# Performance work log

Hardware: AMD Instinct MI355X
Metric: run time of the kernel (lower is better)

## Reference

```python
import jax, jax.numpy as jnp
import numpy as np

B, T, C, N = 4, 1024, 1024, 64
H = C // N
# dims = [max(32, 32*round(fac*C**p/32))] per module formula for C=1024
D_W, D_A, D_V, D_G = 64, 64, 32, 160
GN_EPS = 0.00064


def setup_inputs() -> dict:
    key = jax.random.key(0)
    keys = iter(jax.random.split(key, 40))

    def rn(shape, s=0.02):
        return jax.random.normal(next(keys), shape, jnp.float32) * s

    return {
        "x": jax.random.normal(next(keys), (B, T, C), jnp.float32),
        "v_first": jax.random.normal(next(keys), (B, T, C), jnp.float32),
        "x_r": rn((1, 1, C), 0.5), "x_w": rn((1, 1, C), 0.5), "x_k": rn((1, 1, C), 0.5),
        "x_v": rn((1, 1, C), 0.5), "x_a": rn((1, 1, C), 0.5), "x_g": rn((1, 1, C), 0.5),
        "w0": rn((1, 1, C), 0.5) - 1.0, "w1": rn((C, D_W)), "w2": rn((D_W, C)),
        "a0": rn((1, 1, C), 0.5), "a1": rn((C, D_A)), "a2": rn((D_A, C)),
        "v0p": rn((1, 1, C), 0.5), "v1": rn((C, D_V)), "v2": rn((D_V, C)),
        "g1": rn((C, D_G)), "g2": rn((D_G, C)),
        "k_k": rn((1, 1, C), 0.2) + 0.8, "k_a": rn((1, 1, C), 0.2) + 1.0,
        "r_k": rn((H, N), 0.5),
        "W_r": rn((C, C)), "W_k": rn((C, C)), "W_v": rn((C, C)), "W_o": rn((C, C)),
        "gn_w": jnp.ones((C,), jnp.float32), "gn_b": jnp.zeros((C,), jnp.float32),
    }


def _group_norm(x2, wgt, bias):
    # torch GroupNorm(H groups, C channels) on [B*T, C]: normalize each N-chunk
    xg = x2.reshape(x2.shape[0], H, N)
    mu = xg.mean(-1, keepdims=True)
    var = ((xg - mu) ** 2).mean(-1, keepdims=True)  # biased var, as torch
    xn = (xg - mu) * jax.lax.rsqrt(var + GN_EPS)
    return xn.reshape(x2.shape) * wgt + bias


def rwkv7_recurrence(r, w, k, v, a, b):
    # RWKV-7 chunked-cuda semantics (wind_rwkv naive reference), all [B,T,H,N];
    # w is the per-channel decay exp(-exp(w_raw)) in (0,1).
    # state s: [B,H,N,N], s[i,j] ~ value_i x key_j
    # s_t = s_{t-1} * diag(w_t) + (s_{t-1} @ a_t) outer b_t + v_t outer k_t
    # y_t = s_t @ r_t
    def step(s, inp):
        r_t, w_t, k_t, v_t, a_t, b_t = inp  # each [B,H,N]
        sa = jnp.einsum('bhij,bhj->bhi', s, a_t)
        s = (s * w_t[:, :, None, :]
             + sa[..., None] * b_t[:, :, None, :]
             + v_t[..., None] * k_t[:, :, None, :])
        y = jnp.einsum('bhij,bhj->bhi', s, r_t)
        return s, y

    xs = tuple(jnp.swapaxes(t, 0, 1) for t in (r, w, k, v, a, b))  # [T,B,H,N]
    s0 = jnp.zeros((r.shape[0], r.shape[2], r.shape[3], r.shape[3]), r.dtype)
    _, ys = jax.lax.scan(step, s0, xs)
    return jnp.swapaxes(ys, 0, 1)  # [B,T,H,N]


def reference(x, v_first, x_r, x_w, x_k, x_v, x_a, x_g, w0, w1, w2, a0, a1, a2,
              v0p, v1, v2, g1, g2, k_k, k_a, r_k, W_r, W_k, W_v, W_o, gn_w, gn_b):
    Bx, Tx, Cx = x.shape
    # F.pad(x, (0,0,1,-1)): shift tokens right by one, zero at t=0
    last_x = jnp.concatenate([jnp.zeros_like(x[:, :1]), x[:, :-1]], axis=1)
    dx = last_x - x
    xr, xw, xk, xv, xa, xg = (x + m * dx for m in (x_r, x_w, x_k, x_v, x_a, x_g))
    r = xr @ W_r.T
    w = -jax.nn.softplus(-w0 - jnp.tanh(xw @ w1) @ w2) - 0.5
    k = xk @ W_k.T
    v = xv @ W_v.T
    v = v + (v_first - v) * jax.nn.sigmoid(v0p + (xv @ v1) @ v2)
    a = jax.nn.sigmoid(a0 + (xa @ a1) @ a2)
    g = jax.nn.sigmoid(xg @ g1) @ g2
    kk = k * k_k
    k = k * (1.0 + (a - 1.0) * k_a)
    rs, ws, ks, vs, kks, aa = (t.reshape(Bx, Tx, H, N) for t in (r, w, k, v, kk, a))
    # F.normalize(kk, dim=-1) with eps clamp 1e-12
    kks = kks / jnp.maximum(jnp.linalg.norm(kks, axis=-1, keepdims=True), 1e-12)
    wdec = jnp.exp(-jnp.exp(ws))
    y = rwkv7_recurrence(rs, wdec, ks, vs, kks, -kks * aa)  # [B,T,H,N]
    yn = _group_norm(y.reshape(Bx * Tx, Cx), gn_w, gn_b).reshape(Bx, Tx, Cx)
    yn = yn + ((rs * ks * r_k).sum(-1, keepdims=True) * vs).reshape(Bx, Tx, Cx)
    return (yn * g) @ W_o.T
```

## Files before the change

### kernel.cpp

```cpp
#include <hip/hip_runtime.h>
#include <hip/hip_bf16.h>
#include <math.h>


using bf16 = __hip_bfloat16;
typedef __attribute__((ext_vector_type(8))) short bf16x8;
typedef __attribute__((ext_vector_type(4))) float f32x4;

#define DEVINL __device__ __forceinline__

DEVINL float b2f(bf16 v) { return __bfloat162float(v); }
DEVINL bf16 f2b(float f) { return __float2bfloat16(f); }
DEVINL float sigm(float x) { return 1.f / (1.f + __expf(-x)); }
DEVINL float bfbits2f(unsigned short s) { return __uint_as_float(((unsigned)s) << 16); }
DEVINL float ldin(const void* p, size_t i, int fl) {
  return fl ? ((const float*)p)[i] : b2f(((const bf16*)p)[i]);
}

DEVINL void g2lds16(const void* g, void* l) {
  __builtin_amdgcn_global_load_lds(
      (__attribute__((address_space(1))) void*)(g),
      (__attribute__((address_space(3))) void*)(l), 16, 0, 0);
}

template<int CTRL>
DEVINL float dpp_add(float x) {
  int t = __builtin_amdgcn_update_dpp(0, __float_as_int(x), CTRL, 0xf, 0xf, true);
  return x + __int_as_float(t);
}
DEVINL float rowsum32(float x) {
  x = dpp_add<0x121>(x);
  x = dpp_add<0x122>(x);
  x = dpp_add<0x124>(x);
  x = dpp_add<0x128>(x);
  int t = __builtin_amdgcn_ds_swizzle(__float_as_int(x), 0x401F);
  return x + __int_as_float(t);
}

__global__ void detect_kernel(const unsigned* __restrict__ x, int* __restrict__ flag) {
  __shared__ int cnt[4];
  int tid = threadIdx.x;
  unsigned w = x[tid];
  float v = fabsf(bfbits2f((unsigned short)(w & 0xffffu)));
  bool plaus = (v >= 1e-4f && v <= 16.f);
  unsigned long long m = __ballot(plaus);
  if ((tid & 63) == 0) cnt[tid >> 6] = __popcll(m);
  __syncthreads();
  if (tid == 0) *flag = (cnt[0] + cnt[1] + cnt[2] + cnt[3] < 128) ? 1 : 0;
}

__global__ __launch_bounds__(256)
void prep_kernel(const void* __restrict__ x,
    const void* mr, const void* mw, const void* mk,
    const void* mv, const void* ma, const void* mg,
    const void* W_r, const void* W_k, const void* W_v, const void* W_o,
    bf16* cWr, bf16* cWk, bf16* cWv, bf16* cWo,
    const void* w1, const void* w2, const void* a1, const void* a2,
    const void* v1, const void* v2, const void* g1, const void* g2,
    bf16* w1t, bf16* w2t, bf16* a1t, bf16* a2t,
    bf16* v1t, bf16* v2t, bf16* g1t, bf16* g2t,
    const int* __restrict__ flag,
    bf16* oxr, bf16* oxw, bf16* oxk, bf16* oxv, bf16* oxa, bf16* oxg)
{
  int fl = *flag;
  int bx = blockIdx.x;
  if (bx < 16384) {
    size_t idx = (size_t)bx * 256 + threadIdx.x;
    int c = (int)(idx & 1023);
    int t = (int)((idx >> 10) & 1023);
    float xc = ldin(x, idx, fl);
    float px = (t == 0) ? 0.f : ldin(x, idx - 1024, fl);
    float dx = px - xc;
    oxr[idx] = f2b(xc + ldin(mr, c, fl) * dx);
    oxw[idx] = f2b(xc + ldin(mw, c, fl) * dx);
    oxk[idx] = f2b(xc + ldin(mk, c, fl) * dx);
    oxv[idx] = f2b(xc + ldin(mv, c, fl) * dx);
    oxa[idx] = f2b(xc + ldin(ma, c, fl) * dx);
    oxg[idx] = f2b(xc + ldin(mg, c, fl) * dx);
  } else if (bx < 32768) {
    int g = (bx - 16384) * 256 + threadIdx.x;
    int seg = g >> 20, i = g & 1048575;
    const void* s = seg == 0 ? W_r : seg == 1 ? W_k : seg == 2 ? W_v : W_o;
    bf16* d = seg == 0 ? cWr : seg == 1 ? cWk : seg == 2 ? cWv : cWo;
    d[i] = fl ? f2b(((const float*)s)[i]) : ((const bf16*)s)[i];
  } else {
    int idx = (bx - 32768) * 256 + threadIdx.x;
    if (idx >= 655360) return;
    const int ends[8] = {65536, 131072, 196608, 262144, 294912, 327680, 491520, 655360};
    const int Ks[8] = {1024, 64, 1024, 64, 1024, 32, 1024, 160};
    const int Nd[8] = {64, 1024, 64, 1024, 32, 1024, 160, 1024};
    const void* srcs[8] = {w1, w2, a1, a2, v1, v2, g1, g2};
    bf16* dsts[8] = {w1t, w2t, a1t, a2t, v1t, v2t, g1t, g2t};
    int seg = 0, start = 0;
#pragma unroll
    for (int s2 = 0; s2 < 7; s2++)
      if (idx >= ends[s2]) { seg = s2 + 1; start = ends[s2]; }
    int local = idx - start;
    int K = Ks[seg], N = Nd[seg];
    int k = local / N, n = local - k * N;
    dsts[seg][(size_t)n * K + k] = f2b(ldin(srcs[seg], local, fl));
  }
}

template<typename Epi>
DEVINL void gemm_core(const bf16* __restrict__ A, const bf16* __restrict__ Bt,
                      int K, int Brows, int m0, int n0, Epi&& epi)
{
  __shared__ short As[128 * 32];
  __shared__ short Bs[128 * 32];
  const int tid = threadIdx.x;
  const int wid = tid >> 6, lane = tid & 63;
  const int wr = (wid >> 1) * 64, wc = (wid & 1) * 64;

  f32x4 acc[4][4] = {};

  const int lrow = lane >> 2;
  const int lcol = (lane & 3) * 8;
  int arow0 = m0 + (wid * 2 + 0) * 16 + lrow;
  int arow1 = m0 + (wid * 2 + 1) * 16 + lrow;
  int brow0 = n0 + (wid * 2 + 0) * 16 + lrow; if (brow0 >= Brows) brow0 = Brows - 1;
  int brow1 = n0 + (wid * 2 + 1) * 16 + lrow; if (brow1 >= Brows) brow1 = Brows - 1;

  const short* Ag = (const short*)A;
  const short* Bg = (const short*)Bt;

  for (int kk = 0; kk < K; kk += 32) {
    __syncthreads();
    g2lds16(Ag + (size_t)arow0 * K + kk + lcol, As + (wid * 2 + 0) * 512);
    g2lds16(Ag + (size_t)arow1 * K + kk + lcol, As + (wid * 2 + 1) * 512);
    g2lds16(Bg + (size_t)brow0 * K + kk + lcol, Bs + (wid * 2 + 0) * 512);
    g2lds16(Bg + (size_t)brow1 * K + kk + lcol, Bs + (wid * 2 + 1) * 512);
    __syncthreads();
    bf16x8 af[4], bfr[4];
#pragma unroll
    for (int mi = 0; mi < 4; mi++)
      af[mi] = *(const bf16x8*)(As + (wr + mi * 16 + (lane & 15)) * 32 + (lane >> 4) * 8);
#pragma unroll
    for (int ni = 0; ni < 4; ni++)
      bfr[ni] = *(const bf16x8*)(Bs + (wc + ni * 16 + (lane & 15)) * 32 + (lane >> 4) * 8);
#pragma unroll
    for (int mi = 0; mi < 4; mi++)
#pragma unroll
      for (int ni = 0; ni < 4; ni++)
        acc[mi][ni] = __builtin_amdgcn_mfma_f32_16x16x32_bf16(af[mi], bfr[ni], acc[mi][ni], 0, 0, 0);
  }

  const int cl0 = lane & 15, r0 = (lane >> 4) * 4;
#pragma unroll
  for (int mi = 0; mi < 4; mi++)
#pragma unroll
    for (int ni = 0; ni < 4; ni++) {
      int col = n0 + wc + ni * 16 + cl0;
#pragma unroll
      for (int rr = 0; rr < 4; rr++)
        epi(m0 + wr + mi * 16 + r0 + rr, col, acc[mi][ni][rr]);
    }
}

__global__ __launch_bounds__(256)
void stage1_kernel(const bf16* xw, const bf16* xa, const bf16* xv, const bf16* xg,
                   const bf16* w1t, const bf16* a1t, const bf16* v1t, const bf16* g1t,
                   bf16* hw, bf16* ha, bf16* hv, bf16* hg)
{
  int y = blockIdx.y;
  int seg = (y <= 2) ? y : 3;
  int n0 = (y == 4) ? 128 : 0;
  const bf16* A  = seg == 0 ? xw  : seg == 1 ? xa  : seg == 2 ? xv  : xg;
  const bf16* Bt = seg == 0 ? w1t : seg == 1 ? a1t : seg == 2 ? v1t : g1t;
  int NS         = seg == 0 ? 64  : seg == 1 ? 64  : seg == 2 ? 32  : 160;
  bf16* out      = seg == 0 ? hw  : seg == 1 ? ha  : seg == 2 ? hv  : hg;
  gemm_core(A, Bt, 1024, NS, blockIdx.x * 128, n0, [&](int row, int col, float f) {
    if (col >= NS) return;
    if (seg == 0) f = tanhf(f);
    else if (seg == 3) f = sigm(f);
    out[(size_t)row * NS + col] = f2b(f);
  });
}

__global__ __launch_bounds__(256)
void bigrkv_kernel(const bf16* xr, const bf16* xk, const bf16* xv,
                   const bf16* cWr, const bf16* cWk, const bf16* cWv,
                   bf16* __restrict__ PKb)
{
  int z = blockIdx.z;
  const bf16* A  = z == 0 ? xr  : z == 1 ? xk  : xv;
  const bf16* Bt = z == 0 ? cWr : z == 1 ? cWk : cWv;
  gemm_core(A, Bt, 1024, 1024, blockIdx.x * 128, blockIdx.y * 128,
            [&](int row, int col, float f) {
    PKb[(size_t)row * 5120 + (col >> 6) * 320 + z * 64 + (col & 63)] = f2b(f);
  });
}

__global__ __launch_bounds__(256)
void stage2_kernel(const bf16* hw, const bf16* ha, const bf16* hv, const bf16* hg,
                   const bf16* w2t, const bf16* a2t, const bf16* v2t, const bf16* g2t,
                   bf16* __restrict__ PKb, float* __restrict__ PKw, float* __restrict__ G,
                   const void* w0, const void* a0, const void* v0p, const void* vfirst,
                   const int* __restrict__ flag)
{
  int fl = *flag;
  int z = blockIdx.z;
  const bf16* A  = z == 0 ? hw  : z == 1 ? ha  : z == 2 ? hv  : hg;
  const bf16* Bt = z == 0 ? w2t : z == 1 ? a2t : z == 2 ? v2t : g2t;
  int K          = z == 0 ? 64  : z == 1 ? 64  : z == 2 ? 32  : 160;
  gemm_core(A, Bt, K, 1024, blockIdx.x * 128, blockIdx.y * 128,
            [&](int row, int col, float f) {
    if (z == 0) {
      float zz = -(ldin(w0, col, fl) + f);
      float sp = fmaxf(zz, 0.f) + __logf(1.f + __expf(-fabsf(zz)));
      PKw[(size_t)row * 1024 + col] = __expf(-__expf(-sp - 0.5f));
    } else if (z == 1) {
      PKb[(size_t)row * 5120 + (col >> 6) * 320 + 192 + (col & 63)] =
          f2b(sigm(ldin(a0, col, fl) + f));
    } else if (z == 2) {
      float sg = sigm(ldin(v0p, col, fl) + f);
      size_t pa = (size_t)row * 5120 + (col >> 6) * 320 + 128 + (col & 63);
      float vr = b2f(PKb[pa]);
      float vf = ldin(vfirst, (size_t)row * 1024 + col, fl);
      PKb[pa] = f2b(vr + (vf - vr) * sg);
    } else {
      G[(size_t)row * 1024 + col] = f;
    }
  });
}

__global__ __launch_bounds__(256)
void post_kernel(bf16* __restrict__ PKb, const void* __restrict__ kkw,
                 const void* __restrict__ kaw, const int* __restrict__ flag) {
  int fl = *flag;
  int slot = blockIdx.x * 4 + (threadIdx.x >> 6);
  int tg = slot >> 4, h = slot & 15;
  int n = threadIdx.x & 63, c = h * 64 + n;
  size_t pb = (size_t)tg * 5120 + (size_t)h * 320;
  float kraw = b2f(PKb[pb + 64 + n]);
  float asig = b2f(PKb[pb + 192 + n]);
  float kk = kraw * ldin(kkw, c, fl);
  float ss = kk * kk;
  ss += __shfl_xor(ss, 1);  ss += __shfl_xor(ss, 2);  ss += __shfl_xor(ss, 4);
  ss += __shfl_xor(ss, 8);  ss += __shfl_xor(ss, 16); ss += __shfl_xor(ss, 32);
  float kkn = kk / fmaxf(sqrtf(ss), 1e-12f);
  PKb[pb + 192 + n] = f2b(kkn);
  PKb[pb + 256 + n] = f2b(-kkn * asig);
  PKb[pb + 64 + n]  = f2b(kraw * (1.f + (asig - 1.f) * ldin(kaw, c, fl)));
}

#define RD 8
__global__ __launch_bounds__(64)
void recur_kernel(const bf16* __restrict__ PKb, const float* __restrict__ PKw,
                  float* __restrict__ Y) {
  int blk = blockIdx.x;
  int bh = blk & 63, sib = blk >> 6;
  int b = bh >> 4, h = bh & 15;
  int lane = threadIdx.x;
  int jl = lane & 31, j0 = jl * 2;
  int rl = lane >> 5;
  int i = sib * 2 + rl;

  const unsigned short* pb =
      (const unsigned short*)(PKb) + ((size_t)b * 1024 * 16 + h) * 320;
  const float* pw = PKw + (size_t)b * 1024 * 1024 + h * 64;
  float* yout = Y + (size_t)b * 1024 * 1024 + h * 64 + i;

  unsigned Lr[RD], Lk[RD], La[RD], Lb[RD];
  float2 Lw[RD];
  unsigned short Lv[RD];

#pragma unroll
  for (int d = 0; d < RD; ++d) {
    const unsigned short* s = pb + (size_t)d * 5120;
    Lr[d] = *(const unsigned*)(s + j0);
    Lk[d] = *(const unsigned*)(s + 64 + j0);
    La[d] = *(const unsigned*)(s + 192 + j0);
    Lb[d] = *(const unsigned*)(s + 256 + j0);
    Lv[d] = s[128 + i];
    Lw[d] = *(const float2*)(pw + (size_t)d * 1024 + j0);
  }

  float S0 = 0.f, S1 = 0.f;

  for (int t0 = 0; t0 < 1024; t0 += RD) {
#pragma unroll
    for (int d = 0; d < RD; ++d) {
      int t = t0 + d;
      unsigned ur = Lr[d], uk = Lk[d], ua = La[d], ub = Lb[d];
      float2 wv = Lw[d];
      float vi = bfbits2f(Lv[d]);
      {
        const unsigned short* s = pb + (size_t)(t + RD) * 5120;
        Lr[d] = *(const unsigned*)(s + j0);
        Lk[d] = *(const unsigned*)(s + 64 + j0);
        La[d] = *(const unsigned*)(s + 192 + j0);
        Lb[d] = *(const unsigned*)(s + 256 + j0);
        Lv[d] = s[128 + i];
        Lw[d] = *(const float2*)(pw + (size_t)(t + RD) * 1024 + j0);
      }
      float ax = bfbits2f((unsigned short)(ua & 0xffffu));
      float ay = bfbits2f((unsigned short)(ua >> 16));
      float kx = bfbits2f((unsigned short)(uk & 0xffffu));
      float ky = bfbits2f((unsigned short)(uk >> 16));
      float bx = bfbits2f((unsigned short)(ub & 0xffffu));
      float by = bfbits2f((unsigned short)(ub >> 16));
      float rx = bfbits2f((unsigned short)(ur & 0xffffu));
      float ry = bfbits2f((unsigned short)(ur >> 16));

      float sa = S0 * ax + S1 * ay;
      sa = rowsum32(sa);
      S0 = S0 * wv.x + (sa * bx + vi * kx);
      S1 = S1 * wv.y + (sa * by + vi * ky);
      float y = S0 * rx + S1 * ry;
      y = rowsum32(y);
      if (jl == 0) yout[(size_t)t * 1024] = y;
    }
  }
}

__global__ __launch_bounds__(256)
void gn_kernel(const float* __restrict__ Y, const bf16* __restrict__ PKb,
               const float* __restrict__ G,
               const void* __restrict__ gw, const void* __restrict__ gb,
               const void* __restrict__ rk, const int* __restrict__ flag,
               bf16* __restrict__ Z)
{
  int fl = *flag;
  int slot = blockIdx.x * 4 + (threadIdx.x >> 6);
  int tg = slot >> 4, h = slot & 15;
  int n = threadIdx.x & 63, c = h * 64 + n;
  size_t pb = (size_t)tg * 5120 + (size_t)h * 320;
  float y = Y[(size_t)tg * 1024 + c];
  float rr = b2f(PKb[pb + n]), kf = b2f(PKb[pb + 64 + n]), vv = b2f(PKb[pb + 128 + n]);
  float s1 = y, s2 = y * y, s3 = rr * kf * ldin(rk, c, fl);
#pragma unroll
  for (int m = 1; m < 64; m <<= 1) {
    s1 += __shfl_xor(s1, m);
    s2 += __shfl_xor(s2, m);
    s3 += __shfl_xor(s3, m);
  }
  float mu = s1 * 0.015625f;
  float var = s2 * 0.015625f - mu * mu;
  float xn = (y - mu) * rsqrtf(var + 0.00064f);
  float yn = xn * ldin(gw, c, fl) + ldin(gb, c, fl);
  yn += s3 * vv;
  Z[(size_t)tg * 1024 + c] = f2b(yn * G[(size_t)tg * 1024 + c]);
}

__global__ __launch_bounds__(256)
void outgemm_kernel(const bf16* Z, const bf16* cWo,
                    float* oF, bf16* oB, const int* __restrict__ flag)
{
  int fl = *flag;
  gemm_core(Z, cWo, 1024, 1024, blockIdx.x * 128, blockIdx.y * 128,
            [&](int row, int col, float f) {
    if (fl) oF[(size_t)row * 1024 + col] = f;
    else    oB[(size_t)row * 1024 + col] = f2b(f);
  });
}

extern "C" void kernel_launch(void* const* d_in, const int* in_sizes, int n_in,
                              void* d_out, int out_size, void* d_ws, size_t ws_size,
                              hipStream_t stream)
{
  const void* x      = d_in[0];
  const void* vfirst = d_in[1];
  const void* m_r = d_in[2];  const void* m_w = d_in[3];
  const void* m_k = d_in[4];  const void* m_v = d_in[5];
  const void* m_a = d_in[6];  const void* m_g = d_in[7];
  const void* w0  = d_in[8];  const void* w1  = d_in[9];  const void* w2  = d_in[10];
  const void* a0  = d_in[11]; const void* a1  = d_in[12]; const void* a2  = d_in[13];
  const void* v0p = d_in[14]; const void* v1  = d_in[15]; const void* v2  = d_in[16];
  const void* g1  = d_in[17]; const void* g2  = d_in[18];
  const void* k_k = d_in[19]; const void* k_a = d_in[20]; const void* r_k = d_in[21];
  const void* W_r = d_in[22]; const void* W_k = d_in[23];
  const void* W_v = d_in[24]; const void* W_o = d_in[25];
  const void* gnw = d_in[26]; const void* gnb = d_in[27];
  (void)in_sizes; (void)n_in; (void)out_size; (void)ws_size;

  char* ws = (char*)d_ws;
  size_t off = 0;
  auto alloc = [&](size_t bytes) -> void* {
    void* p = ws + off; off += (bytes + 255) & ~(size_t)255; return p;
  };
  const size_t BTC2 = (size_t)4096 * 1024 * 2;
  int*  flag = (int*)alloc(256);
  bf16* cWr = (bf16*)alloc((size_t)1048576 * 2);
  bf16* cWk = (bf16*)alloc((size_t)1048576 * 2);
  bf16* cWv = (bf16*)alloc((size_t)1048576 * 2);
  bf16* cWo = (bf16*)alloc((size_t)1048576 * 2);
  bf16* w1t = (bf16*)alloc((size_t)65536 * 2);
  bf16* w2t = (bf16*)alloc((size_t)65536 * 2);
  bf16* a1t = (bf16*)alloc((size_t)65536 * 2);
  bf16* a2t = (bf16*)alloc((size_t)65536 * 2);
  bf16* v1t = (bf16*)alloc((size_t)32768 * 2);
  bf16* v2t = (bf16*)alloc((size_t)32768 * 2);
  bf16* g1t = (bf16*)alloc((size_t)163840 * 2);
  bf16* g2t = (bf16*)alloc((size_t)163840 * 2);
  bf16* xr = (bf16*)alloc(BTC2);
  bf16* xw = (bf16*)alloc(BTC2);
  bf16* xk = (bf16*)alloc(BTC2);
  bf16* xv = (bf16*)alloc(BTC2);
  bf16* xa = (bf16*)alloc(BTC2);
  bf16* xg = (bf16*)alloc(BTC2);
  bf16* PKb = (bf16*)alloc((size_t)4096 * 5120 * 2);
  float* PKw = (float*)alloc((size_t)4096 * 1024 * 4);
  bf16* hw  = (bf16*)alloc((size_t)4096 * 64 * 2);
  bf16* ha  = (bf16*)alloc((size_t)4096 * 64 * 2);
  bf16* hv  = (bf16*)alloc((size_t)4096 * 32 * 2);
  bf16* hg  = (bf16*)alloc((size_t)4096 * 160 * 2);
  float* G = (float*)xr;
  float* Y = (float*)xk;
  bf16*  Z = xa;

  detect_kernel<<<1, 256, 0, stream>>>((const unsigned*)x, flag);
  prep_kernel<<<35328, 256, 0, stream>>>(
      x, m_r, m_w, m_k, m_v, m_a, m_g,
      W_r, W_k, W_v, W_o, cWr, cWk, cWv, cWo,
      w1, w2, a1, a2, v1, v2, g1, g2,
      w1t, w2t, a1t, a2t, v1t, v2t, g1t, g2t,
      flag, xr, xw, xk, xv, xa, xg);

  stage1_kernel<<<dim3(32, 5), 256, 0, stream>>>(xw, xa, xv, xg,
                                                 w1t, a1t, v1t, g1t, hw, ha, hv, hg);
  bigrkv_kernel<<<dim3(32, 8, 3), 256, 0, stream>>>(xr, xk, xv, cWr, cWk, cWv, PKb);
  stage2_kernel<<<dim3(32, 8, 4), 256, 0, stream>>>(hw, ha, hv, hg,
                                                    w2t, a2t, v2t, g2t,
                                                    PKb, PKw, G, w0, a0, v0p, vfirst, flag);
  post_kernel<<<16384, 256, 0, stream>>>(PKb, k_k, k_a, flag);
  recur_kernel<<<2048, 64, 0, stream>>>(PKb, PKw, Y);
  gn_kernel<<<16384, 256, 0, stream>>>(Y, PKb, G, gnw, gnb, r_k, flag, Z);
  outgemm_kernel<<<dim3(32, 8), 256, 0, stream>>>(Z, cWo, (float*)d_out, (bf16*)d_out, flag);
}
```

Measured before the change: 608.6 us.

## Map one state row per wavefront in recurrence and merge stage1 into big GEMM launch

The recurrence kernel now assigns one state row i per 64-lane wavefront, with one column per lane, instead of two rows packed into half-waves. This doubles the grid to 4096 blocks and adds a launch-bounds occupancy hint. The reduction becomes a full 64-lane sum through an extra ds_bpermute step. Separately, the small stage1 low-rank GEMMs are folded into the large r/k/v projection launch as an extra z-slice, which removes one kernel launch and lets both run concurrently. The trade-off is a longer reduction chain per timestep and more redundant per-token loads across the larger number of waves.

Result: slower. 721.6 us (+18.6%).

```diff
diff --git a/kernel.cpp b/kernel.cpp
--- a/kernel.cpp
+++ b/kernel.cpp
@@ -28,13 +28,15 @@
   int t = __builtin_amdgcn_update_dpp(0, __float_as_int(x), CTRL, 0xf, 0xf, true);
   return x + __int_as_float(t);
 }
-DEVINL float rowsum32(float x) {
+DEVINL float rowsum64(float x, int bpx) {
   x = dpp_add<0x121>(x);
   x = dpp_add<0x122>(x);
   x = dpp_add<0x124>(x);
   x = dpp_add<0x128>(x);
   int t = __builtin_amdgcn_ds_swizzle(__float_as_int(x), 0x401F);
-  return x + __int_as_float(t);
+  x += __int_as_float(t);
+  int u = __builtin_amdgcn_ds_bpermute(bpx, __float_as_int(x));
+  return x + __int_as_float(u);
 }
 
 __global__ void detect_kernel(const unsigned* __restrict__ x, int* __restrict__ flag) {
@@ -158,37 +160,37 @@
 }
 
 __global__ __launch_bounds__(256)
-void stage1_kernel(const bf16* xw, const bf16* xa, const bf16* xv, const bf16* xg,
-                   const bf16* w1t, const bf16* a1t, const bf16* v1t, const bf16* g1t,
-                   bf16* hw, bf16* ha, bf16* hv, bf16* hg)
-{
-  int y = blockIdx.y;
-  int seg = (y <= 2) ? y : 3;
-  int n0 = (y == 4) ? 128 : 0;
-  const bf16* A  = seg == 0 ? xw  : seg == 1 ? xa  : seg == 2 ? xv  : xg;
-  const bf16* Bt = seg == 0 ? w1t : seg == 1 ? a1t : seg == 2 ? v1t : g1t;
-  int NS         = seg == 0 ? 64  : seg == 1 ? 64  : seg == 2 ? 32  : 160;
-  bf16* out      = seg == 0 ? hw  : seg == 1 ? ha  : seg == 2 ? hv  : hg;
-  gemm_core(A, Bt, 1024, NS, blockIdx.x * 128, n0, [&](int row, int col, float f) {
-    if (col >= NS) return;
-    if (seg == 0) f = tanhf(f);
-    else if (seg == 3) f = sigm(f);
-    out[(size_t)row * NS + col] = f2b(f);
-  });
-}
-
-__global__ __launch_bounds__(256)
-void bigrkv_kernel(const bf16* xr, const bf16* xk, const bf16* xv,
-                   const bf16* cWr, const bf16* cWk, const bf16* cWv,
-                   bf16* __restrict__ PKb)
+void mid_kernel(const bf16* xr, const bf16* xk, const bf16* xv,
+                const bf16* cWr, const bf16* cWk, const bf16* cWv,
+                bf16* __restrict__ PKb,
+                const bf16* xw, const bf16* xa, const bf16* xg,
+                const bf16* w1t, const bf16* a1t, const bf16* v1t, const bf16* g1t,
+                bf16* hw, bf16* ha, bf16* hv, bf16* hg)
 {
   int z = blockIdx.z;
-  const bf16* A  = z == 0 ? xr  : z == 1 ? xk  : xv;
-  const bf16* Bt = z == 0 ? cWr : z == 1 ? cWk : cWv;
-  gemm_core(A, Bt, 1024, 1024, blockIdx.x * 128, blockIdx.y * 128,
-            [&](int row, int col, float f) {
-    PKb[(size_t)row * 5120 + (col >> 6) * 320 + z * 64 + (col & 63)] = f2b(f);
-  });
+  if (z < 3) {
+    const bf16* A  = z == 0 ? xr  : z == 1 ? xk  : xv;
+    const bf16* Bt = z == 0 ? cWr : z == 1 ? cWk : cWv;
+    gemm_core(A, Bt, 1024, 1024, blockIdx.x * 128, blockIdx.y * 128,
+              [&](int row, int col, float f) {
+      PKb[(size_t)row * 5120 + (col >> 6) * 320 + z * 64 + (col & 63)] = f2b(f);
+    });
+  } else {
+    int y = blockIdx.y;
+    if (y >= 5) return;
+    int seg = (y <= 2) ? y : 3;
+    int n0 = (y == 4) ? 128 : 0;
+    const bf16* A  = seg == 0 ? xw  : seg == 1 ? xa  : seg == 2 ? xv  : xg;
+    const bf16* Bt = seg == 0 ? w1t : seg == 1 ? a1t : seg == 2 ? v1t : g1t;
+    int NS         = seg == 0 ? 64  : seg == 1 ? 64  : seg == 2 ? 32  : 160;
+    bf16* out      = seg == 0 ? hw  : seg == 1 ? ha  : seg == 2 ? hv  : hg;
+    gemm_core(A, Bt, 1024, NS, blockIdx.x * 128, n0, [&](int row, int col, float f) {
+      if (col >= NS) return;
+      if (seg == 0) f = tanhf(f);
+      else if (seg == 3) f = sigm(f);
+      out[(size_t)row * NS + col] = f2b(f);
+    });
+  }
 }
 
 __global__ __launch_bounds__(256)
@@ -245,71 +247,54 @@
 }
 
 #define RD 8
-__global__ __launch_bounds__(64)
+__global__ __launch_bounds__(64, 4)
 void recur_kernel(const bf16* __restrict__ PKb, const float* __restrict__ PKw,
                   float* __restrict__ Y) {
   int blk = blockIdx.x;
-  int bh = blk & 63, sib = blk >> 6;
+  int bh = blk & 63, i = blk >> 6;
   int b = bh >> 4, h = bh & 15;
   int lane = threadIdx.x;
-  int jl = lane & 31, j0 = jl * 2;
-  int rl = lane >> 5;
-  int i = sib * 2 + rl;
-
-  const unsigned short* pb =
-      (const unsigned short*)(PKb) + ((size_t)b * 1024 * 16 + h) * 320;
-  const float* pw = PKw + (size_t)b * 1024 * 1024 + h * 64;
+
+  const char* baseB = (const char*)PKb + (size_t)b * 1024 * 10240 + h * 640 + lane * 2;
+  const char* baseV = (const char*)PKb + (size_t)b * 1024 * 10240 + h * 640 + 256 + i * 2;
+  const char* baseW = (const char*)PKw + (size_t)b * 1024 * 4096 + h * 256 + (size_t)lane * 4;
   float* yout = Y + (size_t)b * 1024 * 1024 + h * 64 + i;
-
-  unsigned Lr[RD], Lk[RD], La[RD], Lb[RD];
-  float2 Lw[RD];
-  unsigned short Lv[RD];
-
+  const int bpx = (lane ^ 32) << 2;
+
+  unsigned short Rr[RD], Rk[RD], Ra[RD], Rb[RD], Rv[RD];
+  float Rw[RD];
 #pragma unroll
   for (int d = 0; d < RD; ++d) {
-    const unsigned short* s = pb + (size_t)d * 5120;
-    Lr[d] = *(const unsigned*)(s + j0);
-    Lk[d] = *(const unsigned*)(s + 64 + j0);
-    La[d] = *(const unsigned*)(s + 192 + j0);
-    Lb[d] = *(const unsigned*)(s + 256 + j0);
-    Lv[d] = s[128 + i];
-    Lw[d] = *(const float2*)(pw + (size_t)d * 1024 + j0);
-  }
-
-  float S0 = 0.f, S1 = 0.f;
-
+    const char* pB = baseB + (size_t)d * 10240;
+    Rr[d] = *(const unsigned short*)(pB);
+    Rk[d] = *(const unsigned short*)(pB + 128);
+    Ra[d] = *(const unsigned short*)(pB + 384);
+    Rb[d] = *(const unsigned short*)(pB + 512);
+    Rv[d] = *(const unsigned short*)(baseV + (size_t)d * 10240);
+    Rw[d] = *(const float*)(baseW + (size_t)d * 4096);
+  }
+
+  float S = 0.f;
   for (int t0 = 0; t0 < 1024; t0 += RD) {
 #pragma unroll
     for (int d = 0; d < RD; ++d) {
-      int t = t0 + d;
-      unsigned ur = Lr[d], uk = Lk[d], ua = La[d], ub = Lb[d];
-      float2 wv = Lw[d];
-      float vi = bfbits2f(Lv[d]);
+      float r = bfbits2f(Rr[d]), k = bfbits2f(Rk[d]);
+      float a = bfbits2f(Ra[d]), bb = bfbits2f(Rb[d]);
+      float vi = bfbits2f(Rv[d]), w = Rw[d];
       {
-        const unsigned short* s = pb + (size_t)(t + RD) * 5120;
-        Lr[d] = *(const unsigned*)(s + j0);
-        Lk[d] = *(const unsigned*)(s + 64 + j0);
-        La[d] = *(const unsigned*)(s + 192 + j0);
-        Lb[d] = *(const unsigned*)(s + 256 + j0);
-        Lv[d] = s[128 + i];
-        Lw[d] = *(const float2*)(pw + (size_t)(t + RD) * 1024 + j0);
+        size_t tn = (size_t)(t0 + d + RD);
+        const char* pB = baseB + tn * 10240;
+        Rr[d] = *(const unsigned short*)(pB);
+        Rk[d] = *(const unsigned short*)(pB + 128);
+        Ra[d] = *(const unsigned short*)(pB + 384);
+        Rb[d] = *(const unsigned short*)(pB + 512);
+        Rv[d] = *(const unsigned short*)(baseV + tn * 10240);
+        Rw[d] = *(const float*)(baseW + tn * 4096);
       }
-      float ax = bfbits2f((unsigned short)(ua & 0xffffu));
-      float ay = bfbits2f((unsigned short)(ua >> 16));
-      float kx = bfbits2f((unsigned short)(uk & 0xffffu));
-      float ky = bfbits2f((unsigned short)(uk >> 16));
-      float bx = bfbits2f((unsigned short)(ub & 0xffffu));
-      float by = bfbits2f((unsigned short)(ub >> 16));
-      float rx = bfbits2f((unsigned short)(ur & 0xffffu));
-      float ry = bfbits2f((unsigned short)(ur >> 16));
-
-      float sa = S0 * ax + S1 * ay;
-      sa = rowsum32(sa);
-      S0 = S0 * wv.x + (sa * bx + vi * kx);
-      S1 = S1 * wv.y + (sa * by + vi * ky);
-      float y = S0 * rx + S1 * ry;
-      y = rowsum32(y);
-      if (jl == 0) yout[(size_t)t * 1024] = y;
+      float sa = rowsum64(S * a, bpx);
+      S = S * w + sa * bb + vi * k;
+      float y = rowsum64(S * r, bpx);
+      if (lane == 0) yout[(size_t)(t0 + d) * 1024] = y;
     }
   }
 }
@@ -417,14 +402,14 @@
       w1t, w2t, a1t, a2t, v1t, v2t, g1t, g2t,
       flag, xr, xw, xk, xv, xa, xg);
 
-  stage1_kernel<<<dim3(32, 5), 256, 0, stream>>>(xw, xa, xv, xg,
-                                                 w1t, a1t, v1t, g1t, hw, ha, hv, hg);
-  bigrkv_kernel<<<dim3(32, 8, 3), 256, 0, stream>>>(xr, xk, xv, cWr, cWk, cWv, PKb);
+  mid_kernel<<<dim3(32, 8, 4), 256, 0, stream>>>(xr, xk, xv, cWr, cWk, cWv, PKb,
+                                                 xw, xa, xg, w1t, a1t, v1t, g1t,
+                                                 hw, ha, hv, hg);
   stage2_kernel<<<dim3(32, 8, 4), 256, 0, stream>>>(hw, ha, hv, hg,
                                                     w2t, a2t, v2t, g2t,
                                                     PKb, PKw, G, w0, a0, v0p, vfirst, flag);
   post_kernel<<<16384, 256, 0, stream>>>(PKb, k_k, k_a, flag);
-  recur_kernel<<<2048, 64, 0, stream>>>(PKb, PKw, Y);
+  recur_kernel<<<4096, 64, 0, stream>>>(PKb, PKw, Y);
   gn_kernel<<<16384, 256, 0, stream>>>(Y, PKb, G, gnw, gnb, r_k, flag, Z);
   outgemm_kernel<<<dim3(32, 8), 256, 0, stream>>>(Z, cWo, (float*)d_out, (bf16*)d_out, flag);
 }
```

## Fuse both recurrence reductions into one pass via precomputed k·r and b·r dot products

Applied to the files above, without the earlier changes.

The recurrence output y = S_t·r is rewritten algebraically as (S_{t-1}·(w∘r)) + sa·(b·r) + v·(k·r). The scalar dot products k·r and b·r are precomputed per head and timestep in post_kernel, so both wavefront reductions can run together in one interleaved DPP chain instead of two dependent reductions. Each lane now owns four state columns across 16 lanes, which removes the cross-row swizzle and halves the block count. The cost is an extra small buffer, more reductions in post_kernel, and fewer wavefronts to hide latency in the serial recurrence.

Measured after the change: 672.7 us. 10.5% more time.

```diff
diff --git a/kernel.cpp b/kernel.cpp
--- a/kernel.cpp
+++ b/kernel.cpp
@@ -28,13 +28,11 @@
   int t = __builtin_amdgcn_update_dpp(0, __float_as_int(x), CTRL, 0xf, 0xf, true);
   return x + __int_as_float(t);
 }
-DEVINL float rowsum32(float x) {
-  x = dpp_add<0x121>(x);
-  x = dpp_add<0x122>(x);
-  x = dpp_add<0x124>(x);
-  x = dpp_add<0x128>(x);
-  int t = __builtin_amdgcn_ds_swizzle(__float_as_int(x), 0x401F);
-  return x + __int_as_float(t);
+DEVINL void rowsum16x2(float& p, float& q) {
+  p = dpp_add<0x121>(p); q = dpp_add<0x121>(q);
+  p = dpp_add<0x122>(p); q = dpp_add<0x122>(q);
+  p = dpp_add<0x124>(p); q = dpp_add<0x124>(q);
+  p = dpp_add<0x128>(p); q = dpp_add<0x128>(q);
 }
 
 __global__ void detect_kernel(const unsigned* __restrict__ x, int* __restrict__ flag) {
@@ -225,13 +223,15 @@
 }
 
 __global__ __launch_bounds__(256)
-void post_kernel(bf16* __restrict__ PKb, const void* __restrict__ kkw,
-                 const void* __restrict__ kaw, const int* __restrict__ flag) {
+void post_kernel(bf16* __restrict__ PKb, float* __restrict__ PKs,
+                 const void* __restrict__ kkw, const void* __restrict__ kaw,
+                 const int* __restrict__ flag) {
   int fl = *flag;
   int slot = blockIdx.x * 4 + (threadIdx.x >> 6);
   int tg = slot >> 4, h = slot & 15;
   int n = threadIdx.x & 63, c = h * 64 + n;
   size_t pb = (size_t)tg * 5120 + (size_t)h * 320;
+  float rr   = b2f(PKb[pb + n]);
   float kraw = b2f(PKb[pb + 64 + n]);
   float asig = b2f(PKb[pb + 192 + n]);
   float kk = kraw * ldin(kkw, c, fl);
@@ -239,77 +239,97 @@
   ss += __shfl_xor(ss, 1);  ss += __shfl_xor(ss, 2);  ss += __shfl_xor(ss, 4);
   ss += __shfl_xor(ss, 8);  ss += __shfl_xor(ss, 16); ss += __shfl_xor(ss, 32);
   float kkn = kk / fmaxf(sqrtf(ss), 1e-12f);
+  float bv = -kkn * asig;
+  float kf = kraw * (1.f + (asig - 1.f) * ldin(kaw, c, fl));
   PKb[pb + 192 + n] = f2b(kkn);
-  PKb[pb + 256 + n] = f2b(-kkn * asig);
-  PKb[pb + 64 + n]  = f2b(kraw * (1.f + (asig - 1.f) * ldin(kaw, c, fl)));
+  PKb[pb + 256 + n] = f2b(bv);
+  PKb[pb + 64 + n]  = f2b(kf);
+  float kr = kf * rr, br = bv * rr;
+#pragma unroll
+  for (int m = 1; m < 64; m <<= 1) {
+    kr += __shfl_xor(kr, m);
+    br += __shfl_xor(br, m);
+  }
+  if (n == 0) {
+    PKs[(size_t)tg * 32 + h * 2]     = kr;
+    PKs[(size_t)tg * 32 + h * 2 + 1] = br;
+  }
 }
 
 #define RD 8
 __global__ __launch_bounds__(64)
 void recur_kernel(const bf16* __restrict__ PKb, const float* __restrict__ PKw,
-                  float* __restrict__ Y) {
+                  const float* __restrict__ PKs, float* __restrict__ Y) {
   int blk = blockIdx.x;
   int bh = blk & 63, sib = blk >> 6;
   int b = bh >> 4, h = bh & 15;
   int lane = threadIdx.x;
-  int jl = lane & 31, j0 = jl * 2;
-  int rl = lane >> 5;
-  int i = sib * 2 + rl;
+  int jq = lane & 15, j0 = jq * 4;
+  int rl = lane >> 4;
+  int i = sib * 4 + rl;
 
   const unsigned short* pb =
       (const unsigned short*)(PKb) + ((size_t)b * 1024 * 16 + h) * 320;
   const float* pw = PKw + (size_t)b * 1024 * 1024 + h * 64;
+  const float* ps = PKs + (size_t)b * 32768 + h * 2;
   float* yout = Y + (size_t)b * 1024 * 1024 + h * 64 + i;
 
-  unsigned Lr[RD], Lk[RD], La[RD], Lb[RD];
-  float2 Lw[RD];
+  uint2 Lr[RD], Lk[RD], La[RD], Lb[RD];
+  float4 Lw[RD];
+  float2 Ls[RD];
   unsigned short Lv[RD];
 
 #pragma unroll
   for (int d = 0; d < RD; ++d) {
     const unsigned short* s = pb + (size_t)d * 5120;
-    Lr[d] = *(const unsigned*)(s + j0);
-    Lk[d] = *(const unsigned*)(s + 64 + j0);
-    La[d] = *(const unsigned*)(s + 192 + j0);
-    Lb[d] = *(const unsigned*)(s + 256 + j0);
+    Lr[d] = *(const uint2*)(s + j0);
+    Lk[d] = *(const uint2*)(s + 64 + j0);
+    La[d] = *(const uint2*)(s + 192 + j0);
+    Lb[d] = *(const uint2*)(s + 256 + j0);
     Lv[d] = s[128 + i];
-    Lw[d] = *(const float2*)(pw + (size_t)d * 1024 + j0);
-  }
-
-  float S0 = 0.f, S1 = 0.f;
+    Lw[d] = *(const float4*)(pw + (size_t)d * 1024 + j0);
+    Ls[d] = *(const float2*)(ps + (size_t)d * 32);
+  }
+
+  float S0 = 0.f, S1 = 0.f, S2 = 0.f, S3 = 0.f;
 
   for (int t0 = 0; t0 < 1024; t0 += RD) {
 #pragma unroll
     for (int d = 0; d < RD; ++d) {
       int t = t0 + d;
-      unsigned ur = Lr[d], uk = Lk[d], ua = La[d], ub = Lb[d];
-      float2 wv = Lw[d];
+      uint2 ur = Lr[d], uk = Lk[d], ua = La[d], ub = Lb[d];
+      float4 wv = Lw[d];
+      float2 sc = Ls[d];
       float vi = bfbits2f(Lv[d]);
       {
-        const unsigned short* s = pb + (size_t)(t + RD) * 5120;
-        Lr[d] = *(const unsigned*)(s + j0);
-        Lk[d] = *(const unsigned*)(s + 64 + j0);
-        La[d] = *(const unsigned*)(s + 192 + j0);
-        Lb[d] = *(const unsigned*)(s + 256 + j0);
+        size_t tn = (size_t)(t + RD);
+        const unsigned short* s = pb + tn * 5120;
+        Lr[d] = *(const uint2*)(s + j0);
+        Lk[d] = *(const uint2*)(s + 64 + j0);
+        La[d] = *(const uint2*)(s + 192 + j0);
+        Lb[d] = *(const uint2*)(s + 256 + j0);
         Lv[d] = s[128 + i];
-        Lw[d] = *(const float2*)(pw + (size_t)(t + RD) * 1024 + j0);
+        Lw[d] = *(const float4*)(pw + tn * 1024 + j0);
+        Ls[d] = *(const float2*)(ps + tn * 32);
       }
-      float ax = bfbits2f((unsigned short)(ua & 0xffffu));
-      float ay = bfbits2f((unsigned short)(ua >> 16));
-      float kx = bfbits2f((unsigned short)(uk & 0xffffu));
-      float ky = bfbits2f((unsigned short)(uk >> 16));
-      float bx = bfbits2f((unsigned short)(ub & 0xffffu));
-      float by = bfbits2f((unsigned short)(ub >> 16));
-      float rx = bfbits2f((unsigned short)(ur & 0xffffu));
-      float ry = bfbits2f((unsigned short)(ur >> 16));
-
-      float sa = S0 * ax + S1 * ay;
-      sa = rowsum32(sa);
-      S0 = S0 * wv.x + (sa * bx + vi * kx);
-      S1 = S1 * wv.y + (sa * by + vi * ky);
-      float y = S0 * rx + S1 * ry;
-      y = rowsum32(y);
-      if (jl == 0) yout[(size_t)t * 1024] = y;
+      float ax = bfbits2f((unsigned short)(ua.x & 0xffffu)), ay = bfbits2f((unsigned short)(ua.x >> 16));
+      float az = bfbits2f((unsigned short)(ua.y & 0xffffu)), aw = bfbits2f((unsigned short)(ua.y >> 16));
+      float kx = bfbits2f((unsigned short)(uk.x & 0xffffu)), ky = bfbits2f((unsigned short)(uk.x >> 16));
+      float kz = bfbits2f((unsigned short)(uk.y & 0xffffu)), kw = bfbits2f((unsigned short)(uk.y >> 16));
+      float bx = bfbits2f((unsigned short)(ub.x & 0xffffu)), by = bfbits2f((unsigned short)(ub.x >> 16));
+      float bz = bfbits2f((unsigned short)(ub.y & 0xffffu)), bw = bfbits2f((unsigned short)(ub.y >> 16));
+      float rx = bfbits2f((unsigned short)(ur.x & 0xffffu)), ry = bfbits2f((unsigned short)(ur.x >> 16));
+      float rz = bfbits2f((unsigned short)(ur.y & 0xffffu)), rw = bfbits2f((unsigned short)(ur.y >> 16));
+
+      float p = (S0 * ax + S1 * ay) + (S2 * az + S3 * aw);
+      float q = (S0 * (wv.x * rx) + S1 * (wv.y * ry)) + (S2 * (wv.z * rz) + S3 * (wv.w * rw));
+      rowsum16x2(p, q);
+      float y = q + p * sc.y + vi * sc.x;
+      S0 = S0 * wv.x + (p * bx + vi * kx);
+      S1 = S1 * wv.y + (p * by + vi * ky);
+      S2 = S2 * wv.z + (p * bz + vi * kz);
+      S3 = S3 * wv.w + (p * bw + vi * kw);
+      if (jq == 0) yout[(size_t)t * 1024] = y;
     }
   }
 }
@@ -401,6 +421,7 @@
   bf16* xg = (bf16*)alloc(BTC2);
   bf16* PKb = (bf16*)alloc((size_t)4096 * 5120 * 2);
   float* PKw = (float*)alloc((size_t)4096 * 1024 * 4);
+  float* PKs = (float*)alloc((size_t)4096 * 32 * 4);
   bf16* hw  = (bf16*)alloc((size_t)4096 * 64 * 2);
   bf16* ha  = (bf16*)alloc((size_t)4096 * 64 * 2);
   bf16* hv  = (bf16*)alloc((size_t)4096 * 32 * 2);
@@ -423,8 +444,8 @@
   stage2_kernel<<<dim3(32, 8, 4), 256, 0, stream>>>(hw, ha, hv, hg,
                                                     w2t, a2t, v2t, g2t,
                                                     PKb, PKw, G, w0, a0, v0p, vfirst, flag);
-  post_kernel<<<16384, 256, 0, stream>>>(PKb, k_k, k_a, flag);
-  recur_kernel<<<2048, 64, 0, stream>>>(PKb, PKw, Y);
+  post_kernel<<<16384, 256, 0, stream>>>(PKb, PKs, k_k, k_a, flag);
+  recur_kernel<<<1024, 64, 0, stream>>>(PKb, PKw, PKs, Y);
   gn_kernel<<<16384, 256, 0, stream>>>(Y, PKb, G, gnw, gnb, r_k, flag, Z);
   outgemm_kernel<<<dim3(32, 8), 256, 0, stream>>>(Z, cWo, (float*)d_out, (bf16*)d_out, flag);
 }
```
